# Performance work log

Hardware: AMD Instinct MI355X
Metric: run time of the kernel (lower is better)

Reference implementation:

```python
import jax, jax.numpy as jnp
import numpy as np

RADIUS = 5
ALPHA = 200.0
N, H, W = 8, 352, 352


def _maxpool5(x):
    # F.max_pool2d(kernel=5, stride=1, padding=2); torch pads with -inf for max pool
    return jax.lax.reduce_window(
        x, -jnp.inf, jax.lax.max,
        window_dimensions=(1, 1, 5, 5), window_strides=(1, 1, 1, 1),
        padding=[(0, 0), (0, 0), (2, 2), (2, 2)])


def setup_inputs() -> dict:
    key = jax.random.key(0)
    k1, k2 = jax.random.split(key)
    pred = jax.random.uniform(k1, (N, 1, H, W), dtype=jnp.float32)
    feat = jax.random.uniform(k2, (N, 3, H, W), dtype=jnp.float32)
    return {"pred": pred, "feat": feat}


def reference(pred, feat):
    # interpolate(pred, scale_factor=1.0) and interpolate(feat, size=pred HxW)
    # are identities here (same spatial size, bilinear align_corners).
    sal_map = pred
    image_ = feat

    # contour mask: dilation - erosion of thresholded saliency
    lbl = (sal_map > 0.5).astype(sal_map.dtype)
    ero = 1.0 - _maxpool5(1.0 - lbl)
    dil = _maxpool5(lbl)
    mask = dil - ero  # (N,1,H,W)

    features = jnp.concatenate([image_, sal_map], axis=1)  # (N,4,H,W)
    n, c, h, w = features.shape
    r = RADIUS
    # zero padding matches F.unfold's implicit zero padding
    fpad = jnp.pad(features, ((0, 0), (0, 0), (r, r), (r, r)))
    center_rgb = features[:, :3]   # (N,3,H,W)
    center_sal = features[:, 3:]   # (N,1,H,W)

    # On-the-fly sliding-window reduction instead of materializing the
    # (N,4,11,11,H,W) unfold tensor. 121 static shifts (fixed small set).
    loss_map = jnp.zeros((n, 1, h, w), dtype=features.dtype)
    for dy in range(2 * r + 1):
        for dx in range(2 * r + 1):
            win = fpad[:, :, dy:dy + h, dx:dx + w]  # (N,4,H,W)
            d_rgb = win[:, :3] - center_rgb
            d_sal = jnp.abs(win[:, 3:] - center_sal)
            wgt = jnp.exp(-ALPHA * jnp.sum(d_rgb * d_rgb, axis=1, keepdims=True))
            loss_map = loss_map + wgt * d_sal

    loss = jnp.sum(loss_map * mask) / (jnp.sum(mask) + 1e-6)
    return loss
```

## Files before the change

### kernel.cpp

```cpp
#include <hip/hip_runtime.h>

#define NB 8
#define HH 352
#define WW 352
#define RAD 5
#define TX 32
#define TY 16
#define LW (TX + 2*RAD)
#define LH (TY + 2*RAD)
#define LSTRIDE 43
#define TILES_X (WW / TX)
#define TILES_Y (HH / TY)
#define NBLK (TILES_X * TILES_Y * NB)

#define RGB_SCALE 16.98644781888824f

typedef float f32x2 __attribute__((ext_vector_type(2)));

__device__ __forceinline__ void tap_pair(float wx, float wy, float wz, float ww,
                                         f32x2 cx, f32x2 cy, f32x2 cz, f32x2 cw,
                                         float& accA, float& accB) {
    f32x2 d0 = cx - wx;
    f32x2 d1 = cy - wy;
    f32x2 d2 = cz - wz;
    f32x2 s  = d0 * d0;
    s += d1 * d1;
    s += d2 * d2;
    f32x2 ds = cw - ww;
    accA = fmaf(__builtin_amdgcn_exp2f(-s.x), fabsf(ds.x), accA);
    accB = fmaf(__builtin_amdgcn_exp2f(-s.y), fabsf(ds.y), accB);
}

__device__ __forceinline__ void tap_scalar(const float4& wn, const float4& c,
                                           float& acc) {
    float d0 = wn.x - c.x, d1 = wn.y - c.y, d2 = wn.z - c.z;
    float s = fmaf(d0, d0, fmaf(d1, d1, d2 * d2));
    float e = __builtin_amdgcn_exp2f(-s);
    acc = fmaf(e, fabsf(wn.w - c.w), acc);
}

template <bool INTERIOR>
__device__ __forceinline__ void compute_mask4(const float4* __restrict__ tile,
                                              int ty, int px0, int gy, int gx0,
                                              float* mask) {
    float cmx[8], cmn[8];
    #pragma unroll
    for (int j = 0; j < 8; ++j) {
        int col = px0 + 3 + j;
        float mx = 0.f, mn = 1.f;
        #pragma unroll
        for (int r = 0; r < 5; ++r) {
            float l = (tile[(ty + 3 + r) * LSTRIDE + col].w > 0.5f) ? 1.f : 0.f;
            mx = fmaxf(mx, l);
            if (INTERIOR) {
                mn = fminf(mn, l);
            } else {
                bool rowv = (unsigned)(gy - 2 + r) < (unsigned)HH;
                mn = fminf(mn, rowv ? l : 1.f);
            }
        }
        cmx[j] = mx;
        if (INTERIOR) {
            cmn[j] = mn;
        } else {
            bool colv = (unsigned)(gx0 - 2 + j) < (unsigned)WW;
            cmn[j] = colv ? mn : 1.f;
        }
    }
    #pragma unroll
    for (int k = 0; k < 4; ++k) {
        float mx = cmx[k], mn = cmn[k];
        #pragma unroll
        for (int j2 = 1; j2 < 5; ++j2) {
            mx = fmaxf(mx, cmx[k + j2]);
            mn = fminf(mn, cmn[k + j2]);
        }
        mask[k] = mx - mn;
    }
}

__global__ __launch_bounds__(256, 4)
void btm_loss_kernel(const float* __restrict__ pred,
                     const float* __restrict__ feat,
                     float2* __restrict__ partials) {
    __shared__ float4 tile[LH * LSTRIDE];
    __shared__ float4 xch[128];
    __shared__ float2 wred[4];

    int bid = blockIdx.x;
    int tx_blk = bid % TILES_X;
    int ty_blk = (bid / TILES_X) % TILES_Y;
    int n = bid / (TILES_X * TILES_Y);

    const int x0 = tx_blk * TX;
    const int y0 = ty_blk * TY;

    const size_t plane = (size_t)HH * WW;
    const float* fr = feat + ((size_t)n * 3 + 0) * plane;
    const float* fg = feat + ((size_t)n * 3 + 1) * plane;
    const float* fb = feat + ((size_t)n * 3 + 2) * plane;
    const float* ps = pred + (size_t)n * plane;

    for (int i = threadIdx.x; i < LH * LW; i += 256) {
        int lr = i / LW;
        int lc = i - lr * LW;
        int gy = y0 + lr - RAD;
        int gx = x0 + lc - RAD;
        float4 v = make_float4(0.f, 0.f, 0.f, 0.f);
        if ((unsigned)gy < (unsigned)HH && (unsigned)gx < (unsigned)WW) {
            int gi = gy * WW + gx;
            v.x = fr[gi] * RGB_SCALE;
            v.y = fg[gi] * RGB_SCALE;
            v.z = fb[gi] * RGB_SCALE;
            v.w = ps[gi];
        }
        tile[lr * LSTRIDE + lc] = v;
    }
    __syncthreads();

    const int t   = threadIdx.x;
    const int g   = t >> 7;
    const int tl  = t & 127;
    const int txq = tl & 7;
    const int ty  = tl >> 3;
    const int px0 = txq * 4;

    float4 c0 = tile[(ty + RAD) * LSTRIDE + (px0 + 0 + RAD)];
    float4 c1 = tile[(ty + RAD) * LSTRIDE + (px0 + 1 + RAD)];
    float4 c2 = tile[(ty + RAD) * LSTRIDE + (px0 + 2 + RAD)];
    float4 c3 = tile[(ty + RAD) * LSTRIDE + (px0 + 3 + RAD)];

    f32x2 c01x = {c0.x, c1.x}, c01y = {c0.y, c1.y}, c01z = {c0.z, c1.z}, c01w = {c0.w, c1.w};
    f32x2 c23x = {c2.x, c3.x}, c23y = {c2.y, c3.y}, c23z = {c2.z, c3.z}, c23w = {c2.w, c3.w};

    float acc0 = 0.f, acc1 = 0.f, acc2 = 0.f, acc3 = 0.f;

    const int dy_lo = g ? 6 : 0;
    const int dy_hi = g ? 11 : 6;
    for (int dy = dy_lo; dy < dy_hi; ++dy) {
        const float4* row = &tile[(ty + dy) * LSTRIDE + px0];
        float4 wv[14];
        #pragma unroll
        for (int j = 0; j < 14; ++j) wv[j] = row[j];

        tap_scalar(wv[0],  c0, acc0);
        tap_scalar(wv[11], c1, acc1);
        tap_scalar(wv[2],  c2, acc2);
        tap_scalar(wv[13], c3, acc3);

        #pragma unroll
        for (int j = 1; j <= 10; ++j)
            tap_pair(wv[j].x, wv[j].y, wv[j].z, wv[j].w,
                     c01x, c01y, c01z, c01w, acc0, acc1);
        #pragma unroll
        for (int j = 3; j <= 12; ++j)
            tap_pair(wv[j].x, wv[j].y, wv[j].z, wv[j].w,
                     c23x, c23y, c23z, c23w, acc2, acc3);
    }

    if (g == 1) xch[tl] = make_float4(acc0, acc1, acc2, acc3);
    __syncthreads();

    float num = 0.f, den = 0.f;
    if (g == 0) {
        float4 o = xch[tl];
        acc0 += o.x; acc1 += o.y; acc2 += o.z; acc3 += o.w;

        const int gy  = y0 + ty;
        const int gx0 = x0 + px0;
        float mask[4];
        bool interior = (tx_blk >= 1) && (tx_blk <= 9) &&
                        (ty_blk >= 1) && (ty_blk <= 20);
        if (interior) compute_mask4<true >(tile, ty, px0, gy, gx0, mask);
        else          compute_mask4<false>(tile, ty, px0, gy, gx0, mask);

        num = fmaf(mask[0], acc0, fmaf(mask[1], acc1,
              fmaf(mask[2], acc2, mask[3] * acc3)));
        den = ((mask[0] + mask[1]) + (mask[2] + mask[3]));
    }

    #pragma unroll
    for (int off = 32; off > 0; off >>= 1) {
        num += __shfl_down(num, off, 64);
        den += __shfl_down(den, off, 64);
    }
    int wid  = t >> 6;
    int lane = t & 63;
    if (lane == 0) wred[wid] = make_float2(num, den);
    __syncthreads();
    if (t == 0) {
        float2 a = wred[0];
        a.x += wred[1].x; a.y += wred[1].y;
        partials[bid] = a;
    }
}

__global__ __launch_bounds__(256)
void btm_finalize_kernel(const float2* __restrict__ partials,
                         float* __restrict__ out) {
    __shared__ float2 wred[4];
    float num = 0.f, den = 0.f;
    for (int i = threadIdx.x; i < NBLK; i += 256) {
        float2 p = partials[i];
        num += p.x;
        den += p.y;
    }
    #pragma unroll
    for (int off = 32; off > 0; off >>= 1) {
        num += __shfl_down(num, off, 64);
        den += __shfl_down(den, off, 64);
    }
    int wid  = threadIdx.x >> 6;
    int lane = threadIdx.x & 63;
    if (lane == 0) wred[wid] = make_float2(num, den);
    __syncthreads();
    if (threadIdx.x == 0) {
        float2 a = wred[0];
        #pragma unroll
        for (int w = 1; w < 4; ++w) { a.x += wred[w].x; a.y += wred[w].y; }
        out[0] = a.x / (a.y + 1e-6f);
    }
}

extern "C" void kernel_launch(void* const* d_in, const int* in_sizes, int n_in,
                              void* d_out, int out_size, void* d_ws, size_t ws_size,
                              hipStream_t stream) {
    const float* pred = (const float*)d_in[0];
    const float* feat = (const float*)d_in[1];
    float* out = (float*)d_out;
    float2* partials = (float2*)d_ws;

    btm_loss_kernel<<<dim3(NBLK), dim3(256), 0, stream>>>(pred, feat, partials);
    btm_finalize_kernel<<<dim3(1), dim3(256), 0, stream>>>(partials, out);
}
```

Baseline: 101.6 us.

## Switch to planar SoA shared tiles, taller tiles, and drop dy split

Shared memory moves from interleaved float4 pixels to four planar channel arrays with stride 44, so each thread reads float4 vectors of consecutive pixels per channel. Tile height doubles to 32 rows, which cuts halo reloads, and each thread now covers all 11 rows instead of splitting them across two thread groups. That removes the cross-group exchange and its extra barrier. The cost is more registers per thread and fewer blocks, so occupancy and load balance may suffer.

```diff
diff --git a/kernel.cpp b/kernel.cpp
--- a/kernel.cpp
+++ b/kernel.cpp
@@ -5,10 +5,11 @@
 #define WW 352
 #define RAD 5
 #define TX 32
-#define TY 16
+#define TY 32
 #define LW (TX + 2*RAD)
 #define LH (TY + 2*RAD)
-#define LSTRIDE 43
+#define SST 44
+#define PLANE (LH * SST)
 #define TILES_X (WW / TX)
 #define TILES_Y (HH / TY)
 #define NBLK (TILES_X * TILES_Y * NB)
@@ -17,30 +18,15 @@
 
 typedef float f32x2 __attribute__((ext_vector_type(2)));
 
-__device__ __forceinline__ void tap_pair(float wx, float wy, float wz, float ww,
-                                         f32x2 cx, f32x2 cy, f32x2 cz, f32x2 cw,
-                                         float& accA, float& accB) {
-    f32x2 d0 = cx - wx;
-    f32x2 d1 = cy - wy;
-    f32x2 d2 = cz - wz;
-    f32x2 s  = d0 * d0;
-    s += d1 * d1;
-    s += d2 * d2;
-    f32x2 ds = cw - ww;
-    accA = fmaf(__builtin_amdgcn_exp2f(-s.x), fabsf(ds.x), accA);
-    accB = fmaf(__builtin_amdgcn_exp2f(-s.y), fabsf(ds.y), accB);
-}
-
-__device__ __forceinline__ void tap_scalar(const float4& wn, const float4& c,
-                                           float& acc) {
-    float d0 = wn.x - c.x, d1 = wn.y - c.y, d2 = wn.z - c.z;
-    float s = fmaf(d0, d0, fmaf(d1, d1, d2 * d2));
-    float e = __builtin_amdgcn_exp2f(-s);
-    acc = fmaf(e, fabsf(wn.w - c.w), acc);
+__device__ __forceinline__ f32x2 lo2(float4 q) { f32x2 r; r.x = q.x; r.y = q.y; return r; }
+__device__ __forceinline__ f32x2 hi2(float4 q) { f32x2 r; r.x = q.z; r.y = q.w; return r; }
+__device__ __forceinline__ f32x2 splat2(float v) { f32x2 r; r.x = v; r.y = v; return r; }
+__device__ __forceinline__ float elem(float4 q, int c) {
+    return c == 0 ? q.x : c == 1 ? q.y : c == 2 ? q.z : q.w;
 }
 
 template <bool INTERIOR>
-__device__ __forceinline__ void compute_mask4(const float4* __restrict__ tile,
+__device__ __forceinline__ void compute_mask4(const float* __restrict__ sms,
                                               int ty, int px0, int gy, int gx0,
                                               float* mask) {
     float cmx[8], cmn[8];
@@ -50,7 +36,7 @@
         float mx = 0.f, mn = 1.f;
         #pragma unroll
         for (int r = 0; r < 5; ++r) {
-            float l = (tile[(ty + 3 + r) * LSTRIDE + col].w > 0.5f) ? 1.f : 0.f;
+            float l = (sms[(ty + 3 + r) * SST + col] > 0.5f) ? 1.f : 0.f;
             mx = fmaxf(mx, l);
             if (INTERIOR) {
                 mn = fminf(mn, l);
@@ -83,15 +69,18 @@
 void btm_loss_kernel(const float* __restrict__ pred,
                      const float* __restrict__ feat,
                      float2* __restrict__ partials) {
-    __shared__ float4 tile[LH * LSTRIDE];
-    __shared__ float4 xch[128];
+    __shared__ __align__(16) float sm[4 * PLANE];
     __shared__ float2 wred[4];
 
-    int bid = blockIdx.x;
-    int tx_blk = bid % TILES_X;
-    int ty_blk = (bid / TILES_X) % TILES_Y;
-    int n = bid / (TILES_X * TILES_Y);
-
+    float* const smr = sm;
+    float* const smg = sm + PLANE;
+    float* const smb = sm + 2 * PLANE;
+    float* const sms = sm + 3 * PLANE;
+
+    const int bid = blockIdx.x;
+    const int tx_blk = bid % TILES_X;
+    const int ty_blk = (bid / TILES_X) % TILES_Y;
+    const int n = bid / (TILES_X * TILES_Y);
     const int x0 = tx_blk * TX;
     const int y0 = ty_blk * TY;
 
@@ -106,91 +95,112 @@
         int lc = i - lr * LW;
         int gy = y0 + lr - RAD;
         int gx = x0 + lc - RAD;
-        float4 v = make_float4(0.f, 0.f, 0.f, 0.f);
+        float r = 0.f, g = 0.f, b = 0.f, s = 0.f;
         if ((unsigned)gy < (unsigned)HH && (unsigned)gx < (unsigned)WW) {
             int gi = gy * WW + gx;
-            v.x = fr[gi] * RGB_SCALE;
-            v.y = fg[gi] * RGB_SCALE;
-            v.z = fb[gi] * RGB_SCALE;
-            v.w = ps[gi];
-        }
-        tile[lr * LSTRIDE + lc] = v;
+            r = fr[gi] * RGB_SCALE;
+            g = fg[gi] * RGB_SCALE;
+            b = fb[gi] * RGB_SCALE;
+            s = ps[gi];
+        }
+        int o = lr * SST + lc;
+        smr[o] = r; smg[o] = g; smb[o] = b; sms[o] = s;
     }
     __syncthreads();
 
     const int t   = threadIdx.x;
-    const int g   = t >> 7;
-    const int tl  = t & 127;
-    const int txq = tl & 7;
-    const int ty  = tl >> 3;
+    const int txq = t & 7;
+    const int ty  = t >> 3;
     const int px0 = txq * 4;
 
-    float4 c0 = tile[(ty + RAD) * LSTRIDE + (px0 + 0 + RAD)];
-    float4 c1 = tile[(ty + RAD) * LSTRIDE + (px0 + 1 + RAD)];
-    float4 c2 = tile[(ty + RAD) * LSTRIDE + (px0 + 2 + RAD)];
-    float4 c3 = tile[(ty + RAD) * LSTRIDE + (px0 + 3 + RAD)];
-
-    f32x2 c01x = {c0.x, c1.x}, c01y = {c0.y, c1.y}, c01z = {c0.z, c1.z}, c01w = {c0.w, c1.w};
-    f32x2 c23x = {c2.x, c3.x}, c23y = {c2.y, c3.y}, c23z = {c2.z, c3.z}, c23w = {c2.w, c3.w};
-
-    float acc0 = 0.f, acc1 = 0.f, acc2 = 0.f, acc3 = 0.f;
-
-    const int dy_lo = g ? 6 : 0;
-    const int dy_hi = g ? 11 : 6;
-    for (int dy = dy_lo; dy < dy_hi; ++dy) {
-        const float4* row = &tile[(ty + dy) * LSTRIDE + px0];
-        float4 wv[14];
-        #pragma unroll
-        for (int j = 0; j < 14; ++j) wv[j] = row[j];
-
-        tap_scalar(wv[0],  c0, acc0);
-        tap_scalar(wv[11], c1, acc1);
-        tap_scalar(wv[2],  c2, acc2);
-        tap_scalar(wv[13], c3, acc3);
-
-        #pragma unroll
-        for (int j = 1; j <= 10; ++j)
-            tap_pair(wv[j].x, wv[j].y, wv[j].z, wv[j].w,
-                     c01x, c01y, c01z, c01w, acc0, acc1);
-        #pragma unroll
-        for (int j = 3; j <= 12; ++j)
-            tap_pair(wv[j].x, wv[j].y, wv[j].z, wv[j].w,
-                     c23x, c23y, c23z, c23w, acc2, acc3);
-    }
-
-    if (g == 1) xch[tl] = make_float4(acc0, acc1, acc2, acc3);
-    __syncthreads();
-
-    float num = 0.f, den = 0.f;
-    if (g == 0) {
-        float4 o = xch[tl];
-        acc0 += o.x; acc1 += o.y; acc2 += o.z; acc3 += o.w;
-
-        const int gy  = y0 + ty;
-        const int gx0 = x0 + px0;
-        float mask[4];
-        bool interior = (tx_blk >= 1) && (tx_blk <= 9) &&
-                        (ty_blk >= 1) && (ty_blk <= 20);
-        if (interior) compute_mask4<true >(tile, ty, px0, gy, gx0, mask);
-        else          compute_mask4<false>(tile, ty, px0, gy, gx0, mask);
-
-        num = fmaf(mask[0], acc0, fmaf(mask[1], acc1,
-              fmaf(mask[2], acc2, mask[3] * acc3)));
-        den = ((mask[0] + mask[1]) + (mask[2] + mask[3]));
-    }
+    f32x2 ncr[4], ncg[4], ncb[4], ncs[4];
+    {
+        const int cb = (ty + RAD) * SST + px0 + RAD;
+        #pragma unroll
+        for (int i = 0; i < 4; ++i) {
+            ncr[i] = splat2(-smr[cb + i]);
+            ncg[i] = splat2(-smg[cb + i]);
+            ncb[i] = splat2(-smb[cb + i]);
+            ncs[i] = splat2(-sms[cb + i]);
+        }
+    }
+
+    float accA[4] = {0.f, 0.f, 0.f, 0.f};
+    float accB[4] = {0.f, 0.f, 0.f, 0.f};
+
+    int ro = ty * SST + px0;
+    for (int dy = 0; dy < 2 * RAD + 1; ++dy, ro += SST) {
+        float4 Rq[4], Gq[4], Bq[4], Sq[4];
+        #pragma unroll
+        for (int q = 0; q < 4; ++q) {
+            Rq[q] = *(const float4*)&smr[ro + 4 * q];
+            Gq[q] = *(const float4*)&smg[ro + 4 * q];
+            Bq[q] = *(const float4*)&smb[ro + 4 * q];
+            Sq[q] = *(const float4*)&sms[ro + 4 * q];
+        }
+
+        #pragma unroll
+        for (int i = 0; i < 4; ++i) {
+            const int bp = (i + 1) >> 1;
+            #pragma unroll
+            for (int j = 0; j < 5; ++j) {
+                const int p = bp + j;
+                f32x2 wr = (p & 1) ? hi2(Rq[p >> 1]) : lo2(Rq[p >> 1]);
+                f32x2 wg = (p & 1) ? hi2(Gq[p >> 1]) : lo2(Gq[p >> 1]);
+                f32x2 wb = (p & 1) ? hi2(Bq[p >> 1]) : lo2(Bq[p >> 1]);
+                f32x2 ws = (p & 1) ? hi2(Sq[p >> 1]) : lo2(Sq[p >> 1]);
+
+                f32x2 d0 = wr + ncr[i];
+                f32x2 ssum = d0 * d0;
+                f32x2 d1 = wg + ncg[i];
+                ssum += d1 * d1;
+                f32x2 d2 = wb + ncb[i];
+                ssum += d2 * d2;
+                f32x2 dsv = ws + ncs[i];
+
+                accA[i] = fmaf(__builtin_amdgcn_exp2f(-ssum.x), fabsf(dsv.x), accA[i]);
+                accB[i] = fmaf(__builtin_amdgcn_exp2f(-ssum.y), fabsf(dsv.y), accB[i]);
+            }
+            {
+                const int ks = (i & 1) ? i : (i + 10);
+                const int q = ks >> 2, c = ks & 3;
+                float d0 = elem(Rq[q], c) + ncr[i].x;
+                float d1 = elem(Gq[q], c) + ncg[i].x;
+                float d2 = elem(Bq[q], c) + ncb[i].x;
+                float s2 = fmaf(d0, d0, fmaf(d1, d1, d2 * d2));
+                accB[i] = fmaf(__builtin_amdgcn_exp2f(-s2),
+                               fabsf(elem(Sq[q], c) + ncs[i].x), accB[i]);
+            }
+        }
+    }
+
+    const int gy  = y0 + ty;
+    const int gx0 = x0 + px0;
+    float mask[4];
+    const bool interior = (tx_blk >= 1) && (tx_blk <= TILES_X - 2) &&
+                          (ty_blk >= 1) && (ty_blk <= TILES_Y - 2);
+    if (interior) compute_mask4<true >(sms, ty, px0, gy, gx0, mask);
+    else          compute_mask4<false>(sms, ty, px0, gy, gx0, mask);
+
+    float num = fmaf(mask[0], accA[0] + accB[0],
+                fmaf(mask[1], accA[1] + accB[1],
+                fmaf(mask[2], accA[2] + accB[2],
+                     mask[3] * (accA[3] + accB[3]))));
+    float den = (mask[0] + mask[1]) + (mask[2] + mask[3]);
 
     #pragma unroll
     for (int off = 32; off > 0; off >>= 1) {
         num += __shfl_down(num, off, 64);
         den += __shfl_down(den, off, 64);
     }
-    int wid  = t >> 6;
-    int lane = t & 63;
+    const int wid  = t >> 6;
+    const int lane = t & 63;
     if (lane == 0) wred[wid] = make_float2(num, den);
     __syncthreads();
     if (t == 0) {
         float2 a = wred[0];
-        a.x += wred[1].x; a.y += wred[1].y;
+        #pragma unroll
+        for (int w = 1; w < 4; ++w) { a.x += wred[w].x; a.y += wred[w].y; }
         partials[bid] = a;
     }
 }
```

After: 101.9 us. Within noise of the previous version (+0.2%).

## Double the tile height and software-pipeline LDS window loads across half-rows

Applied to the files above, without the earlier changes.

The tile grows to 32x32 so each of the 256 threads computes all 11 window rows for its 4 pixels. This removes the two-group dy split, the xch exchange and one barrier. The LDS window reads are broken into 7-element halves with double buffering (b0/b1) and sched_barrier, so each load overlaps the exp/FMA work on the previous half. Centre values are pre-negated so differences become adds. The change halves the block count and enlarges the halo-to-work ratio benefit, but it lowers the number of blocks available to fill the GPU and raises register pressure.

```diff
diff --git a/kernel.cpp b/kernel.cpp
--- a/kernel.cpp
+++ b/kernel.cpp
@@ -5,7 +5,7 @@
 #define WW 352
 #define RAD 5
 #define TX 32
-#define TY 16
+#define TY 32
 #define LW (TX + 2*RAD)
 #define LH (TY + 2*RAD)
 #define LSTRIDE 43
@@ -17,40 +17,46 @@
 
 typedef float f32x2 __attribute__((ext_vector_type(2)));
 
-__device__ __forceinline__ void tap_pair(float wx, float wy, float wz, float ww,
-                                         f32x2 cx, f32x2 cy, f32x2 cz, f32x2 cw,
-                                         float& accA, float& accB) {
-    f32x2 d0 = cx - wx;
-    f32x2 d1 = cy - wy;
-    f32x2 d2 = cz - wz;
+struct Half { float4 w[7]; };
+
+__device__ __forceinline__ void load_half(Half& b, const float4* __restrict__ trow,
+                                          int cidx ) {
+    #pragma unroll
+    for (int j = 0; j < 7; ++j) b.w[j] = trow[cidx + j];
+}
+
+__device__ __forceinline__ void tap_pair(const float4& w,
+                                         f32x2 ncx, f32x2 ncy, f32x2 ncz, f32x2 ncw,
+                                         float& aL, float& aH) {
+    f32x2 d0 = ncx + w.x;
+    f32x2 d1 = ncy + w.y;
+    f32x2 d2 = ncz + w.z;
     f32x2 s  = d0 * d0;
     s += d1 * d1;
     s += d2 * d2;
-    f32x2 ds = cw - ww;
-    accA = fmaf(__builtin_amdgcn_exp2f(-s.x), fabsf(ds.x), accA);
-    accB = fmaf(__builtin_amdgcn_exp2f(-s.y), fabsf(ds.y), accB);
-}
-
-__device__ __forceinline__ void tap_scalar(const float4& wn, const float4& c,
-                                           float& acc) {
-    float d0 = wn.x - c.x, d1 = wn.y - c.y, d2 = wn.z - c.z;
+    f32x2 ds = ncw + w.w;
+    aL = fmaf(__builtin_amdgcn_exp2f(-s.x), fabsf(ds.x), aL);
+    aH = fmaf(__builtin_amdgcn_exp2f(-s.y), fabsf(ds.y), aH);
+}
+
+__device__ __forceinline__ void tap_scalar(const float4& w,
+                                           float ncx, float ncy, float ncz, float ncw,
+                                           float& a) {
+    float d0 = w.x + ncx, d1 = w.y + ncy, d2 = w.z + ncz;
     float s = fmaf(d0, d0, fmaf(d1, d1, d2 * d2));
-    float e = __builtin_amdgcn_exp2f(-s);
-    acc = fmaf(e, fabsf(wn.w - c.w), acc);
+    a = fmaf(__builtin_amdgcn_exp2f(-s), fabsf(w.w + ncw), a);
 }
 
 template <bool INTERIOR>
-__device__ __forceinline__ void compute_mask4(const float4* __restrict__ tile,
-                                              int ty, int px0, int gy, int gx0,
-                                              float* mask) {
+__device__ __forceinline__ void compute_mask4(const float4* __restrict__ trow,
+                                              int gy, int gx0, float* mask) {
     float cmx[8], cmn[8];
     #pragma unroll
     for (int j = 0; j < 8; ++j) {
-        int col = px0 + 3 + j;
         float mx = 0.f, mn = 1.f;
         #pragma unroll
         for (int r = 0; r < 5; ++r) {
-            float l = (tile[(ty + 3 + r) * LSTRIDE + col].w > 0.5f) ? 1.f : 0.f;
+            float l = (trow[(3 + r) * LSTRIDE + 3 + j].w > 0.5f) ? 1.f : 0.f;
             mx = fmaxf(mx, l);
             if (INTERIOR) {
                 mn = fminf(mn, l);
@@ -84,14 +90,12 @@
                      const float* __restrict__ feat,
                      float2* __restrict__ partials) {
     __shared__ float4 tile[LH * LSTRIDE];
-    __shared__ float4 xch[128];
     __shared__ float2 wred[4];
 
-    int bid = blockIdx.x;
-    int tx_blk = bid % TILES_X;
-    int ty_blk = (bid / TILES_X) % TILES_Y;
-    int n = bid / (TILES_X * TILES_Y);
-
+    const int bid = blockIdx.x;
+    const int tx_blk = bid % TILES_X;
+    const int ty_blk = (bid / TILES_X) % TILES_Y;
+    const int n = bid / (TILES_X * TILES_Y);
     const int x0 = tx_blk * TX;
     const int y0 = ty_blk * TY;
 
@@ -119,78 +123,87 @@
     __syncthreads();
 
     const int t   = threadIdx.x;
-    const int g   = t >> 7;
-    const int tl  = t & 127;
-    const int txq = tl & 7;
-    const int ty  = tl >> 3;
+    const int txq = t & 7;
+    const int ty  = t >> 3;
     const int px0 = txq * 4;
 
-    float4 c0 = tile[(ty + RAD) * LSTRIDE + (px0 + 0 + RAD)];
-    float4 c1 = tile[(ty + RAD) * LSTRIDE + (px0 + 1 + RAD)];
-    float4 c2 = tile[(ty + RAD) * LSTRIDE + (px0 + 2 + RAD)];
-    float4 c3 = tile[(ty + RAD) * LSTRIDE + (px0 + 3 + RAD)];
-
-    f32x2 c01x = {c0.x, c1.x}, c01y = {c0.y, c1.y}, c01z = {c0.z, c1.z}, c01w = {c0.w, c1.w};
-    f32x2 c23x = {c2.x, c3.x}, c23y = {c2.y, c3.y}, c23z = {c2.z, c3.z}, c23w = {c2.w, c3.w};
+    const float4* trow = tile + ty * LSTRIDE + px0;
+
+    float4 c0 = trow[RAD * LSTRIDE + RAD + 0];
+    float4 c1 = trow[RAD * LSTRIDE + RAD + 1];
+    float4 c2 = trow[RAD * LSTRIDE + RAD + 2];
+    float4 c3 = trow[RAD * LSTRIDE + RAD + 3];
+    f32x2 n01x = {-c0.x, -c1.x}, n01y = {-c0.y, -c1.y}, n01z = {-c0.z, -c1.z}, n01w = {-c0.w, -c1.w};
+    f32x2 n23x = {-c2.x, -c3.x}, n23y = {-c2.y, -c3.y}, n23z = {-c2.z, -c3.z}, n23w = {-c2.w, -c3.w};
 
     float acc0 = 0.f, acc1 = 0.f, acc2 = 0.f, acc3 = 0.f;
 
-    const int dy_lo = g ? 6 : 0;
-    const int dy_hi = g ? 11 : 6;
-    for (int dy = dy_lo; dy < dy_hi; ++dy) {
-        const float4* row = &tile[(ty + dy) * LSTRIDE + px0];
-        float4 wv[14];
-        #pragma unroll
-        for (int j = 0; j < 14; ++j) wv[j] = row[j];
-
-        tap_scalar(wv[0],  c0, acc0);
-        tap_scalar(wv[11], c1, acc1);
-        tap_scalar(wv[2],  c2, acc2);
-        tap_scalar(wv[13], c3, acc3);
-
-        #pragma unroll
-        for (int j = 1; j <= 10; ++j)
-            tap_pair(wv[j].x, wv[j].y, wv[j].z, wv[j].w,
-                     c01x, c01y, c01z, c01w, acc0, acc1);
-        #pragma unroll
-        for (int j = 3; j <= 12; ++j)
-            tap_pair(wv[j].x, wv[j].y, wv[j].z, wv[j].w,
-                     c23x, c23y, c23z, c23w, acc2, acc3);
-    }
-
-    if (g == 1) xch[tl] = make_float4(acc0, acc1, acc2, acc3);
-    __syncthreads();
-
-    float num = 0.f, den = 0.f;
-    if (g == 0) {
-        float4 o = xch[tl];
-        acc0 += o.x; acc1 += o.y; acc2 += o.z; acc3 += o.w;
-
-        const int gy  = y0 + ty;
-        const int gx0 = x0 + px0;
-        float mask[4];
-        bool interior = (tx_blk >= 1) && (tx_blk <= 9) &&
-                        (ty_blk >= 1) && (ty_blk <= 20);
-        if (interior) compute_mask4<true >(tile, ty, px0, gy, gx0, mask);
-        else          compute_mask4<false>(tile, ty, px0, gy, gx0, mask);
-
-        num = fmaf(mask[0], acc0, fmaf(mask[1], acc1,
-              fmaf(mask[2], acc2, mask[3] * acc3)));
-        den = ((mask[0] + mask[1]) + (mask[2] + mask[3]));
-    }
+    auto comp_lo = [&](const Half& b) {
+        tap_scalar(b.w[0], n01x.x, n01y.x, n01z.x, n01w.x, acc0);
+        #pragma unroll
+        for (int j = 1; j <= 6; ++j) tap_pair(b.w[j], n01x, n01y, n01z, n01w, acc0, acc1);
+        tap_scalar(b.w[2], n23x.x, n23y.x, n23z.x, n23w.x, acc2);
+        #pragma unroll
+        for (int j = 3; j <= 6; ++j) tap_pair(b.w[j], n23x, n23y, n23z, n23w, acc2, acc3);
+    };
+    auto comp_hi = [&](const Half& b) {
+        #pragma unroll
+        for (int j = 0; j <= 3; ++j) tap_pair(b.w[j], n01x, n01y, n01z, n01w, acc0, acc1);
+        tap_scalar(b.w[4], n01x.y, n01y.y, n01z.y, n01w.y, acc1);
+        #pragma unroll
+        for (int j = 0; j <= 5; ++j) tap_pair(b.w[j], n23x, n23y, n23z, n23w, acc2, acc3);
+        tap_scalar(b.w[6], n23x.y, n23y.y, n23z.y, n23w.y, acc3);
+    };
+
+    Half b0, b1;
+    load_half(b0, trow, 0);
+
+    #define STEP(H, BC, BP)                                                       \
+        do {                                                                      \
+            if ((H) + 1 < 22)                                                     \
+                load_half(BP, trow, ((((H)+1) >> 1) * LSTRIDE + (((H)+1) & 1) * 7)); \
+            __builtin_amdgcn_sched_barrier(0);                                    \
+            if ((H) & 1) comp_hi(BC); else comp_lo(BC);                           \
+        } while (0)
+
+    STEP(0,  b0, b1);  STEP(1,  b1, b0);
+    STEP(2,  b0, b1);  STEP(3,  b1, b0);
+    STEP(4,  b0, b1);  STEP(5,  b1, b0);
+    STEP(6,  b0, b1);  STEP(7,  b1, b0);
+    STEP(8,  b0, b1);  STEP(9,  b1, b0);
+    STEP(10, b0, b1);  STEP(11, b1, b0);
+    STEP(12, b0, b1);  STEP(13, b1, b0);
+    STEP(14, b0, b1);  STEP(15, b1, b0);
+    STEP(16, b0, b1);  STEP(17, b1, b0);
+    STEP(18, b0, b1);  STEP(19, b1, b0);
+    STEP(20, b0, b1);  STEP(21, b1, b0);
+    #undef STEP
+
+    const int gy  = y0 + ty;
+    const int gx0 = x0 + px0;
+    float mask[4];
+    const bool interior = (tx_blk >= 1) && (tx_blk <= TILES_X - 2) &&
+                          (ty_blk >= 1) && (ty_blk <= TILES_Y - 2);
+    if (interior) compute_mask4<true >(trow, gy, gx0, mask);
+    else          compute_mask4<false>(trow, gy, gx0, mask);
+
+    float num = fmaf(mask[0], acc0, fmaf(mask[1], acc1,
+                fmaf(mask[2], acc2, mask[3] * acc3)));
+    float den = (mask[0] + mask[1]) + (mask[2] + mask[3]);
 
     #pragma unroll
     for (int off = 32; off > 0; off >>= 1) {
         num += __shfl_down(num, off, 64);
         den += __shfl_down(den, off, 64);
     }
-    int wid  = t >> 6;
-    int lane = t & 63;
+    const int wid  = t >> 6;
+    const int lane = t & 63;
     if (lane == 0) wred[wid] = make_float2(num, den);
     __syncthreads();
     if (t == 0) {
         float2 a = wred[0];
-        a.x += wred[1].x; a.y += wred[1].y;
+        #pragma unroll
+        for (int w = 1; w < 4; ++w) { a.x += wred[w].x; a.y += wred[w].y; }
         partials[bid] = a;
     }
 }
```

Result: slower. 302.9 us (+198.0%).
